# Kernel tuning notes

Hardware: AMD Instinct MI355X
Metric: run time of the kernel (lower is better)

## Reference

```python
import jax, jax.numpy as jnp
import numpy as np

LMAX = 3

def make_i2l(lmax):
    # [(lmax+1)^2, lmax+1] 0/1 indicator mapping irrep index -> degree l
    i2l = np.zeros(((lmax + 1) ** 2, lmax + 1), dtype=np.float32)
    count = 0
    for l in range(lmax + 1):
        i2l[count:count + 2 * l + 1, l] = 1.0
        count += 2 * l + 1
    return jnp.asarray(i2l)

def setup_inputs() -> dict:
    key = jax.random.key(0)
    x = jax.random.normal(key, (32, 512, 16, 128), dtype=jnp.float32)  # [b, n, irrep, c]
    i2l = make_i2l(LMAX)
    return {"x": x, "i2l": i2l}

def reference(x, i2l):
    # degree-wise squared norm per neighbor: [b, n, l, c]
    dot = x * x
    ll2 = jnp.einsum('bnic,il->bnlc', dot, i2l)
    # argmax over neighbors, keepdim -> [b, 1, l, c]
    idx = jnp.argmax(ll2, axis=1, keepdims=True)
    # broadcast degree-wise winner index back to irrep components: [b, 1, irrep, c]
    idx_i = jnp.einsum('belc,il->beic', idx.astype(x.dtype), i2l).astype(jnp.int32)
    # gather winning neighbor per (irrep, channel), squeeze neighbor dim -> [b, irrep, c]
    out = jnp.take_along_axis(x, idx_i, axis=1)[:, 0]
    return out
```

## Files before the change

### kernel.cpp

```cpp
#include <hip/hip_runtime.h>
#include <stdint.h>


constexpr int B_  = 32;
constexpr int N_  = 512;
constexpr int IR_ = 16;
constexpr int C_  = 128;
constexpr int NL_ = 4;
constexpr int E_  = NL_ * C_;

constexpr int NCHUNK = 32;
constexpr int CHN    = N_ / NCHUNK;
constexpr int NROW   = 4;
constexpr int NN     = CHN / NROW;

__device__ constexpr int L_OF_I[16] = {0, 1,1,1, 2,2,2,2,2, 3,3,3,3,3,3,3};
__device__ constexpr int I0_OF_L[4] = {0, 1, 4, 9};
__device__ constexpr int NI_OF_L[4] = {1, 3, 5, 7};

__global__ __launch_bounds__(128)
void cmp_phase1(const float* __restrict__ x, unsigned long long* __restrict__ ws) {
    const int t    = threadIdx.x;
    const int c4   = t & 31;
    const int nrow = t >> 5;
    const int chunk = blockIdx.x;
    const int b     = blockIdx.y;

    unsigned long long best[NL_][4];
#pragma unroll
    for (int l = 0; l < NL_; ++l)
#pragma unroll
        for (int j = 0; j < 4; ++j) best[l][j] = 0ull;

    const int n0 = chunk * CHN + nrow * NN;
    const float4* __restrict__ x4 = (const float4*)x;

#pragma unroll
    for (int nn = 0; nn < NN; ++nn) {
        const int n = n0 + nn;
        const long base = ((long)(b * N_ + n) * IR_) * 32 + c4;

        float4 acc[NL_];
#pragma unroll
        for (int l = 0; l < NL_; ++l) { acc[l].x = acc[l].y = acc[l].z = acc[l].w = 0.f; }

#pragma unroll
        for (int i = 0; i < IR_; ++i) {
            const float4 v = x4[base + i * 32];
            const int l = L_OF_I[i];
            acc[l].x += v.x * v.x;
            acc[l].y += v.y * v.y;
            acc[l].z += v.z * v.z;
            acc[l].w += v.w * v.w;
        }

        const unsigned long long code = (unsigned long long)(~(unsigned int)n);
#pragma unroll
        for (int l = 0; l < NL_; ++l) {
            const float vals[4] = {acc[l].x, acc[l].y, acc[l].z, acc[l].w};
#pragma unroll
            for (int j = 0; j < 4; ++j) {
                const unsigned long long p =
                    ((unsigned long long)__float_as_uint(vals[j]) << 32) | code;
                if (p > best[l][j]) best[l][j] = p;
            }
        }
    }

    __shared__ unsigned long long red[NROW][E_];
#pragma unroll
    for (int l = 0; l < NL_; ++l)
#pragma unroll
        for (int j = 0; j < 4; ++j)
            red[nrow][l * C_ + c4 * 4 + j] = best[l][j];
    __syncthreads();

    unsigned long long* __restrict__ wsp = ws + ((long)chunk * B_ + b) * E_;
#pragma unroll
    for (int k = 0; k < 4; ++k) {
        const int e = t + k * 128;
        unsigned long long m = red[0][e];
#pragma unroll
        for (int nr = 1; nr < NROW; ++nr) {
            const unsigned long long v = red[nr][e];
            if (v > m) m = v;
        }
        wsp[e] = m;
    }
}

__global__ __launch_bounds__(128)
void cmp_phase2(const float* __restrict__ x,
                const unsigned long long* __restrict__ ws,
                float* __restrict__ out) {
    const int c = threadIdx.x;
    const int b = blockIdx.x;
    const int l = blockIdx.y;
    const int e = l * C_ + c;

    unsigned long long m = 0ull;
#pragma unroll
    for (int chunk = 0; chunk < NCHUNK; ++chunk) {
        const unsigned long long v = ws[((long)chunk * B_ + b) * E_ + e];
        if (v > m) m = v;
    }
    const int n = (int)(~(unsigned int)(m & 0xFFFFFFFFull));

    const int i0 = I0_OF_L[l];
    const int ni = NI_OF_L[l];
    const long src = (((long)b * N_ + n) * IR_ + i0) * C_ + c;
    const long dst = ((long)b * IR_ + i0) * C_ + c;
#pragma unroll 7
    for (int k = 0; k < ni; ++k) {
        out[dst + (long)k * C_] = x[src + (long)k * C_];
    }
}

extern "C" void kernel_launch(void* const* d_in, const int* in_sizes, int n_in,
                              void* d_out, int out_size, void* d_ws, size_t ws_size,
                              hipStream_t stream) {
    const float* x = (const float*)d_in[0];
    unsigned long long* ws = (unsigned long long*)d_ws;
    float* out = (float*)d_out;

    dim3 g1(NCHUNK, B_);
    cmp_phase1<<<g1, 128, 0, stream>>>(x, ws);
    dim3 g2(B_, NL_);
    cmp_phase2<<<g2, 128, 0, stream>>>(x, ws, out);
}
```

Baseline: 188.8 us.

## Assign one neighbor per thread row and reduce via cross-half-wave shuffle

Phase 1 now uses 256-thread blocks and 64 chunks. Each 32-lane row handles a single neighbor instead of looping over four, so every thread issues all 16 loads at once with no serial dependency. The two half-waves are combined with a 64-bit xor shuffle before the shared-memory reduction across four waves. This raises memory-level parallelism and block count for the bandwidth-bound pass, at the cost of twice as many partial results to write and for phase 2 to read.

```diff
diff --git a/kernel.cpp b/kernel.cpp
--- a/kernel.cpp
+++ b/kernel.cpp
@@ -9,80 +9,73 @@
 constexpr int NL_ = 4;
 constexpr int E_  = NL_ * C_;
 
-constexpr int NCHUNK = 32;
+constexpr int NCHUNK = 64;
 constexpr int CHN    = N_ / NCHUNK;
-constexpr int NROW   = 4;
-constexpr int NN     = CHN / NROW;
 
 __device__ constexpr int L_OF_I[16] = {0, 1,1,1, 2,2,2,2,2, 3,3,3,3,3,3,3};
 __device__ constexpr int I0_OF_L[4] = {0, 1, 4, 9};
 __device__ constexpr int NI_OF_L[4] = {1, 3, 5, 7};
 
-__global__ __launch_bounds__(128)
+__global__ __launch_bounds__(256)
 void cmp_phase1(const float* __restrict__ x, unsigned long long* __restrict__ ws) {
     const int t    = threadIdx.x;
     const int c4   = t & 31;
     const int nrow = t >> 5;
+    const int wv   = t >> 6;
     const int chunk = blockIdx.x;
     const int b     = blockIdx.y;
 
-    unsigned long long best[NL_][4];
+    const int n = chunk * CHN + nrow;
+    const float4* __restrict__ p = (const float4*)x + ((unsigned)(b * N_ + n) * IR_) * 32u + c4;
+
+    float4 acc[NL_];
 #pragma unroll
-    for (int l = 0; l < NL_; ++l)
-#pragma unroll
-        for (int j = 0; j < 4; ++j) best[l][j] = 0ull;
-
-    const int n0 = chunk * CHN + nrow * NN;
-    const float4* __restrict__ x4 = (const float4*)x;
+    for (int l = 0; l < NL_; ++l) { acc[l].x = acc[l].y = acc[l].z = acc[l].w = 0.f; }
 
 #pragma unroll
-    for (int nn = 0; nn < NN; ++nn) {
-        const int n = n0 + nn;
-        const long base = ((long)(b * N_ + n) * IR_) * 32 + c4;
+    for (int i = 0; i < IR_; ++i) {
+        const float4 v = p[i * 32];
+        const int l = L_OF_I[i];
+        acc[l].x += v.x * v.x;
+        acc[l].y += v.y * v.y;
+        acc[l].z += v.z * v.z;
+        acc[l].w += v.w * v.w;
+    }
 
-        float4 acc[NL_];
+    const unsigned long long code = (unsigned long long)(~(unsigned int)n);
+    unsigned long long best[NL_ * 4];
 #pragma unroll
-        for (int l = 0; l < NL_; ++l) { acc[l].x = acc[l].y = acc[l].z = acc[l].w = 0.f; }
+    for (int l = 0; l < NL_; ++l) {
+        const float vals[4] = {acc[l].x, acc[l].y, acc[l].z, acc[l].w};
+#pragma unroll
+        for (int j = 0; j < 4; ++j)
+            best[l * 4 + j] = ((unsigned long long)__float_as_uint(vals[j]) << 32) | code;
+    }
 
 #pragma unroll
-        for (int i = 0; i < IR_; ++i) {
-            const float4 v = x4[base + i * 32];
-            const int l = L_OF_I[i];
-            acc[l].x += v.x * v.x;
-            acc[l].y += v.y * v.y;
-            acc[l].z += v.z * v.z;
-            acc[l].w += v.w * v.w;
-        }
-
-        const unsigned long long code = (unsigned long long)(~(unsigned int)n);
-#pragma unroll
-        for (int l = 0; l < NL_; ++l) {
-            const float vals[4] = {acc[l].x, acc[l].y, acc[l].z, acc[l].w};
-#pragma unroll
-            for (int j = 0; j < 4; ++j) {
-                const unsigned long long p =
-                    ((unsigned long long)__float_as_uint(vals[j]) << 32) | code;
-                if (p > best[l][j]) best[l][j] = p;
-            }
-        }
+    for (int e = 0; e < NL_ * 4; ++e) {
+        const unsigned long long q = __shfl_xor(best[e], 32, 64);
+        if (q > best[e]) best[e] = q;
     }
 
-    __shared__ unsigned long long red[NROW][E_];
+    __shared__ unsigned long long red[4][E_];
+    if ((t & 32) == 0) {
 #pragma unroll
-    for (int l = 0; l < NL_; ++l)
+        for (int l = 0; l < NL_; ++l)
 #pragma unroll
-        for (int j = 0; j < 4; ++j)
-            red[nrow][l * C_ + c4 * 4 + j] = best[l][j];
+            for (int j = 0; j < 4; ++j)
+                red[wv][l * C_ + c4 * 4 + j] = best[l * 4 + j];
+    }
     __syncthreads();
 
     unsigned long long* __restrict__ wsp = ws + ((long)chunk * B_ + b) * E_;
 #pragma unroll
-    for (int k = 0; k < 4; ++k) {
-        const int e = t + k * 128;
+    for (int k = 0; k < 2; ++k) {
+        const int e = t + k * 256;
         unsigned long long m = red[0][e];
 #pragma unroll
-        for (int nr = 1; nr < NROW; ++nr) {
-            const unsigned long long v = red[nr][e];
+        for (int w = 1; w < 4; ++w) {
+            const unsigned long long v = red[w][e];
             if (v > m) m = v;
         }
         wsp[e] = m;
@@ -124,7 +117,7 @@
     float* out = (float*)d_out;
 
     dim3 g1(NCHUNK, B_);
-    cmp_phase1<<<g1, 128, 0, stream>>>(x, ws);
+    cmp_phase1<<<g1, 256, 0, stream>>>(x, ws);
     dim3 g2(B_, NL_);
     cmp_phase2<<<g2, 128, 0, stream>>>(x, ws, out);
 }
```

New measurement: 195.5 us. 1.04x slower.
